# Performance work log

Hardware: AMD Instinct MI355X
Metric: run time of the kernel (lower is better)

The kernel has to match this reference:

```python
import jax, jax.numpy as jnp
import numpy as np

T, B, D = 2048, 4, 1024

def setup_inputs() -> dict:
    key = jax.random.key(0)
    ks = jax.random.split(key, 4)
    return {
        "query": jax.random.normal(ks[0], (T, B, D), jnp.float32),
        "input_feature": jax.random.normal(ks[1], (T, B, D), jnp.float32),
        "in_proj_weight": jax.random.normal(ks[2], (2 * D, D), jnp.float32) * (D ** -0.5),
        "in_proj_bias": jnp.zeros((2 * D,), jnp.float32),
        "out_proj_weight": jax.random.normal(ks[3], (D, D), jnp.float32) * (D ** -0.5),
        "out_proj_bias": jnp.zeros((D,), jnp.float32),
    }

def reference(query, input_feature, in_proj_weight, in_proj_bias, out_proj_weight, out_proj_bias):
    d = query.shape[-1]
    scaling = d ** -0.5
    # joint KV projection: [T,B,2D], then chunk
    kv = jnp.einsum('tbd,ed->tbe', input_feature, in_proj_weight) + in_proj_bias
    k, v = kv[..., :d], kv[..., d:]
    q = query * scaling
    # attn_weights: [B, T(query), S(key)]
    attn_weights = jnp.einsum('tbd,sbd->bts', q, k)
    attn_weights = jax.nn.softmax(attn_weights.astype(jnp.float32), axis=-1).astype(q.dtype)
    # attn: [B,T,D] -> [T,B,D]
    attn = jnp.einsum('bts,sbd->tbd', attn_weights, v)
    attn = jnp.einsum('tbd,ed->tbe', attn, out_proj_weight) + out_proj_bias
    return attn, attn_weights
```

## Files before the change

kernel.cpp:

```cpp
#include <hip/hip_runtime.h>
#include <hip/hip_bf16.h>
#include <type_traits>

static constexpr int T = 2048;
static constexpr int B = 4;
static constexpr int D = 1024;
static constexpr int E = 2 * D;
static constexpr int M1 = T * B;

typedef __attribute__((ext_vector_type(8))) short short8;
typedef __attribute__((ext_vector_type(4))) float f32x4;

__device__ inline ushort f2bf(float x) {
    __hip_bfloat16 h = __float2bfloat16(x);
    return __builtin_bit_cast(ushort, h);
}

__device__ inline void glds16(const void* g, void* l) {
    __builtin_amdgcn_global_load_lds(
        (const __attribute__((address_space(1))) void*)g,
        (__attribute__((address_space(3))) void*)l, 16, 0, 0);
}

template <typename OT>
__global__ __launch_bounds__(256) void mfma_gemm_nt(
    const ushort* __restrict__ A, const ushort* __restrict__ Bt,
    OT* __restrict__ C, const float* __restrict__ bias,
    int K, int lda, int ldb, int ldc,
    long long aBatch, long long bBatch, long long cBatch, float alpha)
{
    __shared__ ushort As[128 * 32];
    __shared__ ushort Bs[128 * 32];

    const int tid  = threadIdx.x;
    const int lane = tid & 63;
    const int wave = tid >> 6;
    const int wm = (wave & 1) * 64;
    const int wn = (wave >> 1) * 64;

    const int bm = blockIdx.y * 128;
    const int bn = blockIdx.x * 128;
    A  += blockIdx.z * aBatch;
    Bt += blockIdx.z * bBatch;
    C  += blockIdx.z * cBatch;

    f32x4 acc[4][4] = {};

    const int srow = lane >> 2;
    const int sElem = (((lane & 3) ^ ((lane >> 3) & 3))) * 8;
    const int rElem = ((lane >> 4) ^ ((lane >> 1) & 3)) * 8;

    for (int k0 = 0; k0 < K; k0 += 32) {
        __syncthreads();
#pragma unroll
        for (int j = 0; j < 2; ++j) {
            const int r = wave * 32 + j * 16 + srow;
            glds16(Bt + (long long)(bn + r) * ldb + (k0 + sElem),
                   (void*)&Bs[wave * 1024 + j * 512]);
            glds16(A + (long long)(bm + r) * lda + (k0 + sElem),
                   (void*)&As[wave * 1024 + j * 512]);
        }
        __syncthreads();

        short8 af[4], bf[4];
#pragma unroll
        for (int i = 0; i < 4; ++i) {
            const int m = wm + i * 16 + (lane & 15);
            af[i] = *(const short8*)&As[m * 32 + rElem];
        }
#pragma unroll
        for (int j = 0; j < 4; ++j) {
            const int n = wn + j * 16 + (lane & 15);
            bf[j] = *(const short8*)&Bs[n * 32 + rElem];
        }
#pragma unroll
        for (int i = 0; i < 4; ++i)
#pragma unroll
            for (int j = 0; j < 4; ++j)
                acc[i][j] = __builtin_amdgcn_mfma_f32_16x16x32_bf16(af[i], bf[j], acc[i][j], 0, 0, 0);
    }

#pragma unroll
    for (int j = 0; j < 4; ++j) {
        const int col = bn + wn + j * 16 + (lane & 15);
        const float bv = bias ? bias[col] : 0.0f;
#pragma unroll
        for (int i = 0; i < 4; ++i) {
            const int row0 = bm + wm + i * 16 + ((lane >> 4) << 2);
#pragma unroll
            for (int r = 0; r < 4; ++r) {
                const float v = acc[i][j][r] * alpha + bv;
                if constexpr (std::is_same<OT, float>::value)
                    C[(long long)(row0 + r) * ldc + col] = v;
                else
                    C[(long long)(row0 + r) * ldc + col] = f2bf(v);
            }
        }
    }
}

__global__ __launch_bounds__(256) void cast_bf16(const float* __restrict__ in,
                                                 ushort* __restrict__ out, int n4)
{
    const int i = blockIdx.x * 256 + threadIdx.x;
    if (i >= n4) return;
    const float4 v = ((const float4*)in)[i];
    ushort4 o;
    o.x = f2bf(v.x); o.y = f2bf(v.y); o.z = f2bf(v.z); o.w = f2bf(v.w);
    ((ushort4*)out)[i] = o;
}

__global__ __launch_bounds__(256) void transpose_v(const ushort* __restrict__ kv,
                                                   ushort* __restrict__ vt)
{
    __shared__ ushort tile[64][65];
    const int s0 = blockIdx.x * 64, d0 = blockIdx.y * 64, b = blockIdx.z;
    const int t = threadIdx.x;
    const int dl = (t & 15) * 4, sl = t >> 4;
#pragma unroll
    for (int p = 0; p < 4; ++p) {
        const int s = sl + p * 16;
        const ushort4 v = *(const ushort4*)&kv[((long long)(s0 + s) * B + b) * E + D + d0 + dl];
        tile[s][dl + 0] = v.x; tile[s][dl + 1] = v.y;
        tile[s][dl + 2] = v.z; tile[s][dl + 3] = v.w;
    }
    __syncthreads();
    const int dl2 = t >> 4, sl2 = (t & 15) * 4;
#pragma unroll
    for (int p = 0; p < 4; ++p) {
        const int d = dl2 + p * 16;
        ushort4 o;
        o.x = tile[sl2 + 0][d]; o.y = tile[sl2 + 1][d];
        o.z = tile[sl2 + 2][d]; o.w = tile[sl2 + 3][d];
        *(ushort4*)&vt[(long long)b * D * T + (long long)(d0 + d) * T + s0 + sl2] = o;
    }
}

__global__ __launch_bounds__(256) void softmax_kernel(float* __restrict__ W,
                                                      ushort* __restrict__ Pbf)
{
    const long long row = blockIdx.x;
    float* p = W + row * (long long)T;
    ushort* pb = Pbf + row * (long long)T;
    const int tid = threadIdx.x;

    float4 v0 = ((const float4*)p)[tid];
    float4 v1 = ((const float4*)p)[tid + 256];

    float m = fmaxf(fmaxf(fmaxf(v0.x, v0.y), fmaxf(v0.z, v0.w)),
                    fmaxf(fmaxf(v1.x, v1.y), fmaxf(v1.z, v1.w)));
#pragma unroll
    for (int off = 1; off < 64; off <<= 1) m = fmaxf(m, __shfl_xor(m, off));

    __shared__ float red[4];
    const int wid = tid >> 6, lane = tid & 63;
    if (lane == 0) red[wid] = m;
    __syncthreads();
    m = fmaxf(fmaxf(red[0], red[1]), fmaxf(red[2], red[3]));
    __syncthreads();

    v0.x = expf(v0.x - m); v0.y = expf(v0.y - m);
    v0.z = expf(v0.z - m); v0.w = expf(v0.w - m);
    v1.x = expf(v1.x - m); v1.y = expf(v1.y - m);
    v1.z = expf(v1.z - m); v1.w = expf(v1.w - m);

    float s = v0.x + v0.y + v0.z + v0.w + v1.x + v1.y + v1.z + v1.w;
#pragma unroll
    for (int off = 1; off < 64; off <<= 1) s += __shfl_xor(s, off);
    if (lane == 0) red[wid] = s;
    __syncthreads();
    s = red[0] + red[1] + red[2] + red[3];

    const float inv = 1.0f / s;
    v0.x *= inv; v0.y *= inv; v0.z *= inv; v0.w *= inv;
    v1.x *= inv; v1.y *= inv; v1.z *= inv; v1.w *= inv;

    ((float4*)p)[tid] = v0;
    ((float4*)p)[tid + 256] = v1;

    ushort4 o0, o1;
    o0.x = f2bf(v0.x); o0.y = f2bf(v0.y); o0.z = f2bf(v0.z); o0.w = f2bf(v0.w);
    o1.x = f2bf(v1.x); o1.y = f2bf(v1.y); o1.z = f2bf(v1.z); o1.w = f2bf(v1.w);
    ((ushort4*)pb)[tid] = o0;
    ((ushort4*)pb)[tid + 256] = o1;
}

extern "C" void kernel_launch(void* const* d_in, const int* in_sizes, int n_in,
                              void* d_out, int out_size, void* d_ws, size_t ws_size,
                              hipStream_t stream)
{
    const float* query = (const float*)d_in[0];
    const float* x     = (const float*)d_in[1];
    const float* w_in  = (const float*)d_in[2];
    const float* b_in  = (const float*)d_in[3];
    const float* w_out = (const float*)d_in[4];
    const float* b_out = (const float*)d_in[5];

    float* out_attn = (float*)d_out;
    float* out_w    = out_attn + (long long)T * B * D;

    char* ws = (char*)d_ws;
    ushort* xbf  = (ushort*)(ws);
    ushort* amid = (ushort*)(ws);
    ushort* qbf  = (ushort*)(ws + (16ll << 20));
    ushort* wibf = (ushort*)(ws + (32ll << 20));
    ushort* wobf = (ushort*)(ws + (36ll << 20));
    ushort* kv   = (ushort*)(ws + (38ll << 20));
    ushort* Pbf  = (ushort*)(ws + (38ll << 20));
    ushort* vt   = (ushort*)(ws + (70ll << 20));

    cast_bf16<<<dim3(8192), 256, 0, stream>>>(x, xbf, (T * B * D) / 4);
    cast_bf16<<<dim3(2048), 256, 0, stream>>>(w_in, wibf, (E * D) / 4);
    cast_bf16<<<dim3(8192), 256, 0, stream>>>(query, qbf, (T * B * D) / 4);
    cast_bf16<<<dim3(1024), 256, 0, stream>>>(w_out, wobf, (D * D) / 4);

    mfma_gemm_nt<ushort><<<dim3(E / 128, M1 / 128, 1), 256, 0, stream>>>(
        xbf, wibf, kv, b_in, D, D, D, E, 0, 0, 0, 1.0f);

    transpose_v<<<dim3(T / 64, D / 64, B), 256, 0, stream>>>(kv, vt);

    mfma_gemm_nt<float><<<dim3(T / 128, T / 128, B), 256, 0, stream>>>(
        qbf, kv, out_w, nullptr, D, B * D, B * E, T,
        (long long)D, (long long)E, (long long)T * T, 0.03125f);

    softmax_kernel<<<dim3(B * T), 256, 0, stream>>>(out_w, Pbf);

    mfma_gemm_nt<ushort><<<dim3(D / 128, T / 128, B), 256, 0, stream>>>(
        Pbf, vt, amid, nullptr, T, T, T, B * D,
        (long long)T * T, (long long)D * T, (long long)D, 1.0f);

    mfma_gemm_nt<float><<<dim3(D / 128, M1 / 128, 1), 256, 0, stream>>>(
        amid, wobf, out_attn, b_out, D, D, D, D, 0, 0, 0, 1.0f);
}
```

Before: 406.4 us.

## Double GEMM K-tile to 64 with new LDS swizzle and fuse cast kernels

The MFMA GEMM now stages 64-wide K slices per iteration instead of 32. This halves the number of barrier pairs and loop iterations and adds a new XOR swizzle for the wider LDS rows. The four separate fp32-to-bf16 cast launches are merged into one kernel that dispatches on block index, removing launch overhead. LDS use per block doubles, which may lower occupancy.

```diff
diff --git a/kernel.cpp b/kernel.cpp
--- a/kernel.cpp
+++ b/kernel.cpp
@@ -29,8 +29,8 @@
     int K, int lda, int ldb, int ldc,
     long long aBatch, long long bBatch, long long cBatch, float alpha)
 {
-    __shared__ ushort As[128 * 32];
-    __shared__ ushort Bs[128 * 32];
+    __shared__ ushort As[128 * 64];
+    __shared__ ushort Bs[128 * 64];
 
     const int tid  = threadIdx.x;
     const int lane = tid & 63;
@@ -46,38 +46,43 @@
 
     f32x4 acc[4][4] = {};
 
-    const int srow = lane >> 2;
-    const int sElem = (((lane & 3) ^ ((lane >> 3) & 3))) * 8;
-    const int rElem = ((lane >> 4) ^ ((lane >> 1) & 3)) * 8;
-
-    for (int k0 = 0; k0 < K; k0 += 32) {
+    const int srow  = lane >> 3;
+    const int sElem = (((lane & 7) ^ (lane >> 3))) * 8;
+    const int rbase = ((lane >> 4) ^ (lane & 7)) * 8;
+    const int rxor4 = 4 * 8;
+
+    for (int k0 = 0; k0 < K; k0 += 64) {
         __syncthreads();
 #pragma unroll
-        for (int j = 0; j < 2; ++j) {
-            const int r = wave * 32 + j * 16 + srow;
-            glds16(Bt + (long long)(bn + r) * ldb + (k0 + sElem),
-                   (void*)&Bs[wave * 1024 + j * 512]);
-            glds16(A + (long long)(bm + r) * lda + (k0 + sElem),
-                   (void*)&As[wave * 1024 + j * 512]);
+        for (int j = 0; j < 4; ++j) {
+            const int r = wave * 32 + j * 8;
+            glds16(Bt + (long long)(bn + r + srow) * ldb + (k0 + sElem),
+                   (void*)&Bs[r * 64]);
+            glds16(A + (long long)(bm + r + srow) * lda + (k0 + sElem),
+                   (void*)&As[r * 64]);
         }
         __syncthreads();
 
-        short8 af[4], bf[4];
-#pragma unroll
-        for (int i = 0; i < 4; ++i) {
-            const int m = wm + i * 16 + (lane & 15);
-            af[i] = *(const short8*)&As[m * 32 + rElem];
+#pragma unroll
+        for (int kb = 0; kb < 2; ++kb) {
+            const int rElem = rbase ^ (kb ? rxor4 : 0);
+            short8 af[4], bf[4];
+#pragma unroll
+            for (int i = 0; i < 4; ++i) {
+                const int m = wm + i * 16 + (lane & 15);
+                af[i] = *(const short8*)&As[m * 64 + rElem];
+            }
+#pragma unroll
+            for (int j = 0; j < 4; ++j) {
+                const int n = wn + j * 16 + (lane & 15);
+                bf[j] = *(const short8*)&Bs[n * 64 + rElem];
+            }
+#pragma unroll
+            for (int i = 0; i < 4; ++i)
+#pragma unroll
+                for (int j = 0; j < 4; ++j)
+                    acc[i][j] = __builtin_amdgcn_mfma_f32_16x16x32_bf16(af[i], bf[j], acc[i][j], 0, 0, 0);
         }
-#pragma unroll
-        for (int j = 0; j < 4; ++j) {
-            const int n = wn + j * 16 + (lane & 15);
-            bf[j] = *(const short8*)&Bs[n * 32 + rElem];
-        }
-#pragma unroll
-        for (int i = 0; i < 4; ++i)
-#pragma unroll
-            for (int j = 0; j < 4; ++j)
-                acc[i][j] = __builtin_amdgcn_mfma_f32_16x16x32_bf16(af[i], bf[j], acc[i][j], 0, 0, 0);
     }
 
 #pragma unroll
@@ -99,15 +104,23 @@
     }
 }
 
-__global__ __launch_bounds__(256) void cast_bf16(const float* __restrict__ in,
-                                                 ushort* __restrict__ out, int n4)
-{
-    const int i = blockIdx.x * 256 + threadIdx.x;
-    if (i >= n4) return;
-    const float4 v = ((const float4*)in)[i];
+__global__ __launch_bounds__(256) void cast_all(
+    const float* __restrict__ s0, ushort* __restrict__ d0, int n0,
+    const float* __restrict__ s1, ushort* __restrict__ d1, int n1,
+    const float* __restrict__ s2, ushort* __restrict__ d2, int n2,
+    const float* __restrict__ s3, ushort* __restrict__ d3, int n3)
+{
+    int blk = blockIdx.x;
+    const float* s; ushort* d;
+    if (blk < n0) { s = s0; d = d0; }
+    else if ((blk -= n0) < n1) { s = s1; d = d1; }
+    else if ((blk -= n1) < n2) { s = s2; d = d2; }
+    else { blk -= n2; s = s3; d = d3; }
+    const int i = blk * 256 + threadIdx.x;
+    const float4 v = ((const float4*)s)[i];
     ushort4 o;
     o.x = f2bf(v.x); o.y = f2bf(v.y); o.z = f2bf(v.z); o.w = f2bf(v.w);
-    ((ushort4*)out)[i] = o;
+    ((ushort4*)d)[i] = o;
 }
 
 __global__ __launch_bounds__(256) void transpose_v(const ushort* __restrict__ kv,
@@ -209,10 +222,8 @@
     ushort* Pbf  = (ushort*)(ws + (38ll << 20));
     ushort* vt   = (ushort*)(ws + (70ll << 20));
 
-    cast_bf16<<<dim3(8192), 256, 0, stream>>>(x, xbf, (T * B * D) / 4);
-    cast_bf16<<<dim3(2048), 256, 0, stream>>>(w_in, wibf, (E * D) / 4);
-    cast_bf16<<<dim3(8192), 256, 0, stream>>>(query, qbf, (T * B * D) / 4);
-    cast_bf16<<<dim3(1024), 256, 0, stream>>>(w_out, wobf, (D * D) / 4);
+    cast_all<<<dim3(8192 + 2048 + 8192 + 1024), 256, 0, stream>>>(
+        x, xbf, 8192, w_in, wibf, 2048, query, qbf, 8192, w_out, wobf, 1024);
 
     mfma_gemm_nt<ushort><<<dim3(E / 128, M1 / 128, 1), 256, 0, stream>>>(
         xbf, wibf, kv, b_in, D, D, D, E, 0, 0, 0, 1.0f);
```

New measurement: 357.9 us. 11.9% less time.
